# Kernel optimization log

Measured on AMD Instinct MI355X. Metric: run time of the kernel, lower is better.

The kernel has to match this reference:

```python
import jax, jax.numpy as jnp
import numpy as np

B, C, H, W = 2, 256, 80, 160
G, P, E = 8, 8, 2  # groups(heads), sampling points, ffn expansion
LN_EPS = 1e-5


def setup_inputs() -> dict:
    key = jax.random.key(0)
    ks = jax.random.split(key, 12)
    def n(k, shape, s=1.0):
        return jax.random.normal(k, shape, dtype=jnp.float32) * s
    return dict(
        feats=n(ks[0], (B, C, H, W)),
        feats_pos=n(ks[1], (B, C, H, W)),
        anchor_points=jax.random.uniform(ks[2], (B, H, W, 2), dtype=jnp.float32),
        value_W=n(ks[3], (C, C), 0.02), value_b=jnp.zeros((C,), jnp.float32),
        off_W=n(ks[4], (C, G * P * 2), 0.02), off_b=n(ks[5], (G * P * 2,), 0.02),
        attn_W=n(ks[6], (C, G * P), 0.02), attn_b=jnp.zeros((G * P,), jnp.float32),
        out_W=n(ks[7], (C, C), 0.02), out_b=jnp.zeros((C,), jnp.float32),
        ln1_g=jnp.ones((C,), jnp.float32), ln1_b=jnp.zeros((C,), jnp.float32),
        ln2_g=jnp.ones((C,), jnp.float32), ln2_b=jnp.zeros((C,), jnp.float32),
        ffn_w1=n(ks[8], (E * C, C), 0.02), ffn_b1=jnp.zeros((E * C,), jnp.float32),
        ffn_w2=n(ks[9], (C, E * C), 0.02), ffn_b2=jnp.zeros((C,), jnp.float32),
    )


def _layernorm(x, g, b):
    m = jnp.mean(x, axis=-1, keepdims=True)
    v = jnp.mean(jnp.square(x - m), axis=-1, keepdims=True)
    return (x - m) * jax.lax.rsqrt(v + LN_EPS) * g + b


def _bilinear_sample(value, px, py, h, w):
    # value: [b,G,HW,cg]; px,py: [b,G,P,HW] pixel coords (align_corners=False)
    x0 = jnp.floor(px); y0 = jnp.floor(py)
    wx1 = px - x0; wx0 = 1.0 - wx1
    wy1 = py - y0; wy0 = 1.0 - wy1
    vexp = value[:, :, None, :, :]  # [b,G,1,HW,cg]
    def gather(xi, yi):
        valid = ((xi >= 0) & (xi < w) & (yi >= 0) & (yi < h)).astype(value.dtype)
        xc = jnp.clip(xi, 0, w - 1).astype(jnp.int32)
        yc = jnp.clip(yi, 0, h - 1).astype(jnp.int32)
        idx = yc * w + xc  # [b,G,P,HW]
        v = jnp.take_along_axis(vexp, idx[..., None], axis=3)  # [b,G,P,HW,cg]
        return v * valid[..., None]
    return (gather(x0, y0) * (wx0 * wy0)[..., None]
            + gather(x0 + 1, y0) * (wx1 * wy0)[..., None]
            + gather(x0, y0 + 1) * (wx0 * wy1)[..., None]
            + gather(x0 + 1, y0 + 1) * (wx1 * wy1)[..., None])


def reference(feats, feats_pos, anchor_points,
              value_W, value_b, off_W, off_b, attn_W, attn_b, out_W, out_b,
              ln1_g, ln1_b, ln2_g, ln2_b, ffn_w1, ffn_b1, ffn_w2, ffn_b2):
    b, c, h, w = feats.shape
    hw = h * w
    cg = c // G
    x = feats + feats_pos                              # residual input (pos-encoded)
    q = x.reshape(b, c, hw).transpose(0, 2, 1)         # [b,HW,c]
    # deformable attention
    val = (q @ value_W + value_b).reshape(b, hw, G, cg).transpose(0, 2, 1, 3)   # [b,G,HW,cg]
    off = (q @ off_W + off_b).reshape(b, hw, G, P, 2).transpose(0, 2, 3, 1, 4)  # [b,G,P,HW,2]
    attn = jax.nn.softmax((q @ attn_W + attn_b).reshape(b, hw, G, P)
                          .transpose(0, 2, 3, 1), axis=2)                        # [b,G,P,HW]
    anchor = anchor_points.reshape(b, hw, 2)[:, None, None, :, :]               # [b,1,1,HW,2]
    loc = anchor + off / jnp.array([w, h], dtype=off.dtype)                     # normalized xy
    px = loc[..., 0] * w - 0.5
    py = loc[..., 1] * h - 0.5
    sampled = _bilinear_sample(val, px, py, h, w)                               # [b,G,P,HW,cg]
    agg = jnp.einsum('bgpn,bgpnc->bngc', attn, sampled).reshape(b, hw, c)
    upd = agg @ out_W + out_b
    # residual + LN1
    y = _layernorm(q + upd, ln1_g, ln1_b)
    # conv1x1 - SiLU - conv1x1 FFN + residual + LN2
    ffn = jax.nn.silu(y @ ffn_w1.T + ffn_b1) @ ffn_w2.T + ffn_b2
    y = _layernorm(y + ffn, ln2_g, ln2_b)
    return y.transpose(0, 2, 1).reshape(b, c, h, w)
```

## Files before the change

kernel.cpp:

```cpp
#include <hip/hip_runtime.h>
#include <hip/hip_bf16.h>
#include <math.h>
#include <stdint.h>

#define B_ 2
#define C_ 256
#define H_ 80
#define W_ 160
#define HW_ (H_*W_)
#define NTOK (B_*HW_)
#define G_ 8
#define P_ 8
#define NQKV 448
#define NQKVP 512
#define PREP_BLOCKS 1794

typedef __bf16 bf16;
typedef __attribute__((ext_vector_type(8))) __bf16 bf16x8;
typedef __attribute__((ext_vector_type(4))) float f32x4;

__device__ __forceinline__ void gload_lds16(const void* g, void* l) {
  __builtin_amdgcn_global_load_lds(
      (__attribute__((address_space(1))) void*)g,
      (__attribute__((address_space(3))) void*)l,
      16, 0, 0);
}

__global__ __launch_bounds__(256)
void prep_kernel(const float* __restrict__ vW, const float* __restrict__ vb,
                 const float* __restrict__ oW, const float* __restrict__ ob,
                 const float* __restrict__ aW, const float* __restrict__ ab,
                 const float* __restrict__ outW,
                 const float* __restrict__ w1, const float* __restrict__ w2,
                 const float* __restrict__ f, const float* __restrict__ fp,
                 bf16* __restrict__ wqkv, float* __restrict__ bqkv,
                 bf16* __restrict__ woutt, bf16* __restrict__ w1b,
                 bf16* __restrict__ w2b, bf16* __restrict__ qb)
{
  __shared__ float lt[64][65];
  const int tid = threadIdx.x;
  const int bid = blockIdx.x;
  if (bid < PREP_BLOCKS) {
    int i = bid * 256 + tid;
    if (i < NQKVP*256) {
      int nn = i >> 8, k = i & 255;
      float w;
      if (nn < 256)      w = vW[k*256 + nn];
      else if (nn < 384) w = oW[k*128 + (nn-256)];
      else if (nn < 448) w = aW[k*64  + (nn-384)];
      else               w = 0.f;
      wqkv[i] = (bf16)w;
    }
    int j = i - NQKVP*256;
    if (j >= 0 && j < 256*256) {
      int nn = j >> 8, k = j & 255;
      woutt[j] = (bf16)outW[k*256 + nn];
    }
    int j2 = i - (NQKVP*256 + 256*256);
    if (j2 >= 0 && j2 < 512*256) w1b[j2] = (bf16)w1[j2];
    int j3 = i - (NQKVP*256 + 256*256 + 512*256);
    if (j3 >= 0 && j3 < 256*512) w2b[j3] = (bf16)w2[j3];
    int j4 = i - (NQKVP*256 + 256*256 + 512*256 + 256*512);
    if (j4 >= 0 && j4 < NQKVP) {
      float bv;
      if (j4 < 256)      bv = vb[j4];
      else if (j4 < 384) bv = ob[j4-256];
      else if (j4 < 448) bv = ab[j4-384];
      else               bv = 0.f;
      bqkv[j4] = bv;
    }
  } else {
    const int b2 = bid - PREP_BLOCKS;
    const int n0 = (b2 % 200) * 64;
    const int c0 = ((b2 / 200) & 3) * 64;
    const int b  = b2 / 800;
#pragma unroll
    for (int i = 0; i < 16; ++i) {
      int cl = i*4 + (tid >> 6), nl = tid & 63;
      size_t gi = ((size_t)(b*C_ + c0 + cl))*HW_ + n0 + nl;
      lt[cl][nl] = f[gi] + fp[gi];
    }
    __syncthreads();
#pragma unroll
    for (int i = 0; i < 16; ++i) {
      int nl = i*4 + (tid >> 6), cl = tid & 63;
      size_t qi = ((size_t)(b*HW_ + n0 + nl))*C_ + c0 + cl;
      qb[qi] = (bf16)lt[cl][nl];
    }
  }
}

template<int EPI, int KTOT>
__global__ __launch_bounds__(256)
void gemm_kernel(const bf16* __restrict__ A, const bf16* __restrict__ Bt,
                 const float* __restrict__ bias,
                 void* __restrict__ out0, float* __restrict__ out1,
                 float* __restrict__ out2)
{
  __shared__ bf16 lA[128*64];
  __shared__ bf16 lB[128*64];
  const int tid  = threadIdx.x;
  const int wave = tid >> 6, lane = tid & 63;
  const int m0 = blockIdx.x * 128, n0 = blockIdx.y * 128;
  const int wm = wave >> 1, wn = wave & 1;
  const int fr = lane & 15;
  const int fq = lane >> 4;
  f32x4 acc[4][4] = {};

  for (int kc = 0; kc < KTOT/64; ++kc) {
    if (kc) __syncthreads();
#pragma unroll
    for (int it = 0; it < 4; ++it) {
      int chunk = it*256 + tid;
      int row = chunk >> 3, cb = chunk & 7;
      int ksw = ((cb ^ (row & 7)) << 3);
      gload_lds16(A  + (size_t)(m0+row)*KTOT + kc*64 + ksw,
                  (char*)lA + it*4096 + wave*1024);
      gload_lds16(Bt + (size_t)(n0+row)*KTOT + kc*64 + ksw,
                  (char*)lB + it*4096 + wave*1024);
    }
    __syncthreads();
#pragma unroll
    for (int ks = 0; ks < 2; ++ks) {
      bf16x8 af[4], bg[4];
#pragma unroll
      for (int i = 0; i < 4; ++i) {
        int ar = wm*64 + i*16 + fr;
        af[i] = *(const bf16x8*)&lA[ar*64 + (((ks*4 + fq) ^ (ar & 7)) << 3)];
        int br = wn*64 + i*16 + fr;
        bg[i] = *(const bf16x8*)&lB[br*64 + (((ks*4 + fq) ^ (br & 7)) << 3)];
      }
#pragma unroll
      for (int mi = 0; mi < 4; ++mi)
#pragma unroll
        for (int ni = 0; ni < 4; ++ni)
          acc[mi][ni] = __builtin_amdgcn_mfma_f32_16x16x32_bf16(af[mi], bg[ni], acc[mi][ni], 0, 0, 0);
    }
  }

#pragma unroll
  for (int mi = 0; mi < 4; ++mi)
#pragma unroll
  for (int ni = 0; ni < 4; ++ni)
#pragma unroll
  for (int r = 0; r < 4; ++r) {
    int row = m0 + wm*64 + mi*16 + fq*4 + r;
    int col = n0 + wn*64 + ni*16 + fr;
    float v = acc[mi][ni][r] + bias[col];
    if (EPI == 0) {
      if (col < 256) {
        int g = col >> 5, ch = col & 31;
        int b = row >= HW_ ? 1 : 0;
        int n = row - b*HW_;
        ((bf16*)out0)[(((size_t)(b*G_ + g))*HW_ + n)*32 + ch] = (bf16)v;
      }
      else if (col < 384) out1[(size_t)row*128 + (col-256)] = v;
      else if (col < 448) out2[(size_t)row*64  + (col-384)] = v;
    } else {
      float s = v / (1.0f + __expf(-v));
      ((bf16*)out0)[(size_t)row*512 + col] = (bf16)s;
    }
  }
}

template<int KTOT, bool NCHW_OUT>
__global__ __launch_bounds__(512)
void gemm_ln64_kernel(const bf16* __restrict__ A, const bf16* __restrict__ Bt,
                      const float* __restrict__ bias, const bf16* __restrict__ res,
                      const float* __restrict__ gg, const float* __restrict__ bb,
                      bf16* __restrict__ yb, float* __restrict__ outf)
{
  __shared__ __align__(16) char smem[40960];
  bf16* lA = (bf16*)smem;
  bf16* lB = (bf16*)(smem + 8192);
  float (*lt)[68] = (float(*)[68])smem;
  __shared__ float2 red[64][4];
  const int tid  = threadIdx.x;
  const int wave = tid >> 6, lane = tid & 63;
  const int m0 = blockIdx.x * 64;
  const int wm = wave >> 2, wn = wave & 3;
  const int fr = lane & 15;
  const int fq = lane >> 4;
  f32x4 acc[2][4] = {};

  for (int kc = 0; kc < KTOT/64; ++kc) {
    if (kc) __syncthreads();
    {
      int row = tid >> 3, cb = tid & 7;
      gload_lds16(A + (size_t)(m0+row)*KTOT + kc*64 + ((cb ^ (row&7))<<3),
                  (char*)lA + wave*1024);
    }
#pragma unroll
    for (int it = 0; it < 4; ++it) {
      int chunk = it*512 + tid;
      int row = chunk >> 3, cb = chunk & 7;
      gload_lds16(Bt + (size_t)row*KTOT + kc*64 + ((cb ^ (row&7))<<3),
                  (char*)lB + it*8192 + wave*1024);
    }
    __syncthreads();
#pragma unroll
    for (int ks = 0; ks < 2; ++ks) {
      bf16x8 af[2], bg[4];
#pragma unroll
      for (int i = 0; i < 2; ++i) {
        int ar = wm*32 + i*16 + fr;
        af[i] = *(const bf16x8*)&lA[ar*64 + (((ks*4 + fq) ^ (ar&7))<<3)];
      }
#pragma unroll
      for (int i = 0; i < 4; ++i) {
        int br = wn*64 + i*16 + fr;
        bg[i] = *(const bf16x8*)&lB[br*64 + (((ks*4 + fq) ^ (br&7))<<3)];
      }
#pragma unroll
      for (int mi = 0; mi < 2; ++mi)
#pragma unroll
        for (int ni = 0; ni < 4; ++ni)
          acc[mi][ni] = __builtin_amdgcn_mfma_f32_16x16x32_bf16(af[mi], bg[ni], acc[mi][ni], 0, 0, 0);
    }
  }

  float gcol[4], bcol[4];
#pragma unroll
  for (int ni = 0; ni < 4; ++ni) {
    int col = wn*64 + ni*16 + fr;
    gcol[ni] = gg[col]; bcol[ni] = bb[col];
  }
#pragma unroll
  for (int mi = 0; mi < 2; ++mi)
#pragma unroll
  for (int r = 0; r < 4; ++r) {
    int rowl = wm*32 + mi*16 + fq*4 + r;
    size_t rowg = (size_t)(m0 + rowl);
    float s = 0.f, q = 0.f;
#pragma unroll
    for (int ni = 0; ni < 4; ++ni) {
      int col = wn*64 + ni*16 + fr;
      float v = acc[mi][ni][r] + bias[col] + (float)res[rowg*256 + col];
      acc[mi][ni][r] = v;
      s += v; q += v*v;
    }
#pragma unroll
    for (int o = 1; o < 16; o <<= 1) { s += __shfl_xor(s, o, 64); q += __shfl_xor(q, o, 64); }
    if (fr == 0) red[rowl][wn] = make_float2(s, q);
  }
  __syncthreads();
#pragma unroll
  for (int mi = 0; mi < 2; ++mi)
#pragma unroll
  for (int r = 0; r < 4; ++r) {
    int rowl = wm*32 + mi*16 + fq*4 + r;
    float s = 0.f, q = 0.f;
#pragma unroll
    for (int k = 0; k < 4; ++k) { float2 p = red[rowl][k]; s += p.x; q += p.y; }
    const float mean = s * (1.f/256.f);
    const float var  = q * (1.f/256.f) - mean*mean;
    const float rs   = rsqrtf(var + 1e-5f);
#pragma unroll
    for (int ni = 0; ni < 4; ++ni)
      acc[mi][ni][r] = (acc[mi][ni][r] - mean)*rs*gcol[ni] + bcol[ni];
  }

  if constexpr (!NCHW_OUT) {
#pragma unroll
    for (int mi = 0; mi < 2; ++mi)
#pragma unroll
    for (int ni = 0; ni < 4; ++ni)
#pragma unroll
    for (int r = 0; r < 4; ++r) {
      size_t rowg = (size_t)(m0 + wm*32 + mi*16 + fq*4 + r);
      int col = wn*64 + ni*16 + fr;
      yb[rowg*256 + col] = (bf16)acc[mi][ni][r];
    }
  } else {
    const int bq = m0 / HW_;
    const int n0 = m0 % HW_;
    __syncthreads();
#pragma unroll
    for (int ch = 0; ch < 4; ++ch) {
      if (ch) __syncthreads();
      if (wn == ch) {
#pragma unroll
        for (int mi = 0; mi < 2; ++mi)
#pragma unroll
        for (int ni = 0; ni < 4; ++ni)
#pragma unroll
        for (int r = 0; r < 4; ++r)
          lt[ni*16 + fr][wm*32 + mi*16 + fq*4 + r] = acc[mi][ni][r];
      }
      __syncthreads();
#pragma unroll
      for (int j = 0; j < 2; ++j) {
        int flat = j*512 + tid;
        int cl = flat >> 4, t4 = (flat & 15) * 4;
        float4 v4 = *(const float4*)&lt[cl][t4];
        *(float4*)&outf[((size_t)(bq*C_ + ch*64 + cl))*HW_ + n0 + t4] = v4;
      }
    }
  }
}

__global__ __launch_bounds__(256)
void sample_kernel(const bf16* __restrict__ val, const float* __restrict__ off,
                   const float* __restrict__ attnl, const float* __restrict__ anchors,
                   bf16* __restrict__ agg)
{
  const int tid  = threadIdx.x;
  const int lane = tid & 63;
  const int wv   = tid >> 6;
  const int c8   = lane & 3;
  const int bid  = blockIdx.x;
  const int g    = bid & 7;
  const int chunk= bid >> 3;
  const int t    = chunk*64 + wv*16 + (lane >> 2);
  const int b    = (t >= HW_) ? 1 : 0;

  const float2 anc = *(const float2*)(anchors + (size_t)t*2);
  const float ax = anc.x * W_ - 0.5f;
  const float ay = anc.y * H_ - 0.5f;

  const float4 l0 = *(const float4*)(attnl + (size_t)t*64 + g*8);
  const float4 l1 = *(const float4*)(attnl + (size_t)t*64 + g*8 + 4);
  float l[8] = {l0.x, l0.y, l0.z, l0.w, l1.x, l1.y, l1.z, l1.w};
  float mx = l[0];
#pragma unroll
  for (int p = 1; p < 8; ++p) mx = fmaxf(mx, l[p]);
  float s = 0.f;
#pragma unroll
  for (int p = 0; p < 8; ++p) { l[p] = __expf(l[p] - mx); s += l[p]; }
  const float inv = 1.f / s;

  const float4* opv = (const float4*)(off + (size_t)t*128 + g*16);
  const float4 o0 = opv[0], o1 = opv[1], o2 = opv[2], o3 = opv[3];
  const float ox[8] = {o0.x, o0.z, o1.x, o1.z, o2.x, o2.z, o3.x, o3.z};
  const float oy[8] = {o0.y, o0.w, o1.y, o1.w, o2.y, o2.w, o3.y, o3.w};

  const bf16* vb = val + ((size_t)(b*G_ + g)*HW_)*32 + c8*8;

  float a[8] = {};
#pragma unroll
  for (int pb = 0; pb < 2; ++pb) {
    float w4[4][4];
    int   ofs[4][4];
#pragma unroll
    for (int pi = 0; pi < 4; ++pi) {
      const int p = pb*4 + pi;
      const float px = ax + ox[p], py = ay + oy[p];
      const float x0f = floorf(px), y0f = floorf(py);
      const int x0 = (int)x0f, y0 = (int)y0f;
      const float wx1 = px - x0f, wx0 = 1.f - wx1;
      const float wy1 = py - y0f, wy0 = 1.f - wy1;
      const float ap = l[p] * inv;
      const bool vx0 = (unsigned)x0 < W_, vx1 = (unsigned)(x0+1) < W_;
      const bool vy0 = (unsigned)y0 < H_, vy1 = (unsigned)(y0+1) < H_;
      w4[pi][0] = (vx0 && vy0) ? ap*wx0*wy0 : 0.f;
      w4[pi][1] = (vx1 && vy0) ? ap*wx1*wy0 : 0.f;
      w4[pi][2] = (vx0 && vy1) ? ap*wx0*wy1 : 0.f;
      w4[pi][3] = (vx1 && vy1) ? ap*wx1*wy1 : 0.f;
      const int xc0 = min(max(x0, 0), W_-1),   xc1 = min(max(x0+1, 0), W_-1);
      const int yc0 = min(max(y0, 0), H_-1),   yc1 = min(max(y0+1, 0), H_-1);
      ofs[pi][0] = (yc0*W_ + xc0)*32;
      ofs[pi][1] = (yc0*W_ + xc1)*32;
      ofs[pi][2] = (yc1*W_ + xc0)*32;
      ofs[pi][3] = (yc1*W_ + xc1)*32;
    }
    bf16x8 v[4][4];
#pragma unroll
    for (int pi = 0; pi < 4; ++pi)
#pragma unroll
      for (int cn = 0; cn < 4; ++cn)
        v[pi][cn] = *(const bf16x8*)(vb + ofs[pi][cn]);
#pragma unroll
    for (int pi = 0; pi < 4; ++pi)
#pragma unroll
      for (int cn = 0; cn < 4; ++cn)
#pragma unroll
        for (int c = 0; c < 8; ++c)
          a[c] += w4[pi][cn] * (float)v[pi][cn][c];
  }
  bf16 r[8];
#pragma unroll
  for (int c = 0; c < 8; ++c) r[c] = (bf16)a[c];
  *(bf16x8*)(agg + (size_t)t*256 + g*32 + c8*8) = *(bf16x8*)r;
}

extern "C" void kernel_launch(void* const* d_in, const int* in_sizes, int n_in,
                              void* d_out, int out_size, void* d_ws, size_t ws_size,
                              hipStream_t stream)
{
  const float* feats   = (const float*)d_in[0];
  const float* featsp  = (const float*)d_in[1];
  const float* anchors = (const float*)d_in[2];
  const float* value_W = (const float*)d_in[3];
  const float* value_b = (const float*)d_in[4];
  const float* off_W   = (const float*)d_in[5];
  const float* off_b   = (const float*)d_in[6];
  const float* attn_W  = (const float*)d_in[7];
  const float* attn_b  = (const float*)d_in[8];
  const float* out_W   = (const float*)d_in[9];
  const float* out_b   = (const float*)d_in[10];
  const float* ln1_g   = (const float*)d_in[11];
  const float* ln1_b   = (const float*)d_in[12];
  const float* ln2_g   = (const float*)d_in[13];
  const float* ln2_b   = (const float*)d_in[14];
  const float* w1      = (const float*)d_in[15];
  const float* b1      = (const float*)d_in[16];
  const float* w2      = (const float*)d_in[17];
  const float* b2      = (const float*)d_in[18];
  float* out = (float*)d_out;

  char* ws = (char*)d_ws;
  size_t cur = 0;
  auto alloc = [&](size_t bytes) -> char* {
    char* p = ws + cur;
    cur += (bytes + 255) & ~(size_t)255;
    return p;
  };
  bf16*  wqkv  = (bf16*) alloc((size_t)NQKVP*256*2);
  bf16*  woutt = (bf16*) alloc((size_t)256*256*2);
  bf16*  w1b   = (bf16*) alloc((size_t)512*256*2);
  bf16*  w2b   = (bf16*) alloc((size_t)256*512*2);
  float* bqkv  = (float*)alloc((size_t)NQKVP*4);
  bf16*  qb    = (bf16*) alloc((size_t)NTOK*256*2);
  bf16*  valb  = (bf16*) alloc((size_t)NTOK*256*2);
  float* offv  = (float*)alloc((size_t)NTOK*128*4);
  float* attnl = (float*)alloc((size_t)NTOK*64*4);
  bf16*  aggb  = (bf16*) alloc((size_t)NTOK*256*2);
  bf16*  y1b   = (bf16*) alloc((size_t)NTOK*256*2);
  bf16*  hb    = (bf16*) alloc((size_t)NTOK*512*2);

  prep_kernel<<<PREP_BLOCKS + 1600, 256, 0, stream>>>(
      value_W, value_b, off_W, off_b, attn_W, attn_b, out_W, w1, w2,
      feats, featsp, wqkv, bqkv, woutt, w1b, w2b, qb);

  gemm_kernel<0, 256><<<dim3(NTOK/128, NQKVP/128), 256, 0, stream>>>(
      qb, wqkv, bqkv, valb, offv, attnl);

  sample_kernel<<<NTOK/8, 256, 0, stream>>>(valb, offv, attnl, anchors, aggb);

  gemm_ln64_kernel<256, false><<<NTOK/64, 512, 0, stream>>>(
      aggb, woutt, out_b, qb, ln1_g, ln1_b, y1b, nullptr);

  gemm_kernel<2, 256><<<dim3(NTOK/128, 512/128), 256, 0, stream>>>(
      y1b, w1b, b1, hb, nullptr, nullptr);

  gemm_ln64_kernel<512, true><<<NTOK/64, 512, 0, stream>>>(
      hb, w2b, b2, y1b, ln2_g, ln2_b, nullptr, out);
}
```

Baseline: 132.1 us.

## Assign sample-kernel work to XCDs by group via atomic work queues

Each sample_kernel block reads its XCC id and atomically claims a chunk from a per-(batch,group) counter, preferring the group matching its XCD. This keeps each attention group's value slice inside one XCD's L2 and avoids scattered gathers across all L2s. It adds global atomics, a block-level sync, and counter reset in the prep kernel. Work stealing happens when a queue is exhausted.

```diff
diff --git a/kernel.cpp b/kernel.cpp
--- a/kernel.cpp
+++ b/kernel.cpp
@@ -35,12 +35,14 @@
                  const float* __restrict__ f, const float* __restrict__ fp,
                  bf16* __restrict__ wqkv, float* __restrict__ bqkv,
                  bf16* __restrict__ woutt, bf16* __restrict__ w1b,
-                 bf16* __restrict__ w2b, bf16* __restrict__ qb)
+                 bf16* __restrict__ w2b, bf16* __restrict__ qb,
+                 int* __restrict__ cnt)
 {
   __shared__ float lt[64][65];
   const int tid = threadIdx.x;
   const int bid = blockIdx.x;
   if (bid < PREP_BLOCKS) {
+    if (bid == 0 && tid < 16) cnt[tid] = 0;
     int i = bid * 256 + tid;
     if (i < NQKVP*256) {
       int nn = i >> 8, k = i & 255;
@@ -302,17 +304,30 @@
 __global__ __launch_bounds__(256)
 void sample_kernel(const bf16* __restrict__ val, const float* __restrict__ off,
                    const float* __restrict__ attnl, const float* __restrict__ anchors,
-                   bf16* __restrict__ agg)
+                   int* __restrict__ cnt, bf16* __restrict__ agg)
 {
+  __shared__ int sq, sc;
   const int tid  = threadIdx.x;
+  if (tid == 0) {
+    uint32_t xcc;
+    asm volatile("s_getreg_b32 %0, hwreg(HW_REG_XCC_ID)" : "=s"(xcc));
+    const int x = (int)(xcc & 7);
+    int q, c, i = 0;
+    for (;;) {
+      q = ((x + (i >> 1)) & 7) | ((i & 1) << 3);
+      c = atomicAdd(&cnt[q], 1);
+      if (c < 200) break;
+      ++i;
+    }
+    sq = q; sc = c;
+  }
+  __syncthreads();
+  const int g = sq & 7;
+  const int b = sq >> 3;
   const int lane = tid & 63;
   const int wv   = tid >> 6;
   const int c8   = lane & 3;
-  const int bid  = blockIdx.x;
-  const int g    = bid & 7;
-  const int chunk= bid >> 3;
-  const int t    = chunk*64 + wv*16 + (lane >> 2);
-  const int b    = (t >= HW_) ? 1 : 0;
+  const int t    = b*HW_ + sc*64 + wv*16 + (lane >> 2);
 
   const float2 anc = *(const float2*)(anchors + (size_t)t*2);
   const float ax = anc.x * W_ - 0.5f;
@@ -415,6 +430,7 @@
     cur += (bytes + 255) & ~(size_t)255;
     return p;
   };
+  int*   cnt   = (int*)  alloc(16*4);
   bf16*  wqkv  = (bf16*) alloc((size_t)NQKVP*256*2);
   bf16*  woutt = (bf16*) alloc((size_t)256*256*2);
   bf16*  w1b   = (bf16*) alloc((size_t)512*256*2);
@@ -430,12 +446,12 @@
 
   prep_kernel<<<PREP_BLOCKS + 1600, 256, 0, stream>>>(
       value_W, value_b, off_W, off_b, attn_W, attn_b, out_W, w1, w2,
-      feats, featsp, wqkv, bqkv, woutt, w1b, w2b, qb);
+      feats, featsp, wqkv, bqkv, woutt, w1b, w2b, qb, cnt);
 
   gemm_kernel<0, 256><<<dim3(NTOK/128, NQKVP/128), 256, 0, stream>>>(
       qb, wqkv, bqkv, valb, offv, attnl);
 
-  sample_kernel<<<NTOK/8, 256, 0, stream>>>(valb, offv, attnl, anchors, aggb);
+  sample_kernel<<<NTOK/8, 256, 0, stream>>>(valb, offv, attnl, anchors, cnt, aggb);
 
   gemm_ln64_kernel<256, false><<<NTOK/64, 512, 0, stream>>>(
       aggb, woutt, out_b, qb, ln1_g, ln1_b, y1b, nullptr);
```

Result: slower. 170.5 us (+29.1%).
